# Kernel optimization log

Measured on AMD Instinct MI355X. Metric: run time of the kernel, lower is better.

The kernel has to match this reference:

```python
import jax, jax.numpy as jnp
import numpy as np

B, N, C, H = 4, 1024, 1024, 16
HD = C // H  # 64
THETA = 10000.0


def _rope_cos_sin(n, hd, theta):
    # classic 1D RoPE cache; [n, hd] with each freq repeated twice (interleaved pairs)
    inv_freq = 1.0 / theta ** (jnp.arange(0, hd, 2, dtype=jnp.float32) / hd)
    t = jnp.arange(n, dtype=jnp.float32)
    freqs = t[:, None] * inv_freq[None, :]              # [n, hd/2]
    cos = jnp.repeat(jnp.cos(freqs), 2, axis=-1)        # [n, hd]
    sin = jnp.repeat(jnp.sin(freqs), 2, axis=-1)
    # original clones & forces row 0 to identity rotation (already true since t=0)
    cos = cos.at[0].set(1.0)
    sin = sin.at[0].set(0.0)
    return cos, sin


def _rotate_half(x):
    # interleaved rotate-half: (x0,x1,x2,x3,...) -> (-x1,x0,-x3,x2,...)
    x1 = x[..., 0::2]
    x2 = x[..., 1::2]
    return jnp.stack((-x2, x1), axis=-1).reshape(x.shape)


def setup_inputs() -> dict:
    key = jax.random.key(0)
    ks = jax.random.split(key, 5)
    s = 0.02
    return {
        "x": jax.random.normal(ks[0], (B, N, C), dtype=jnp.float32),
        "qkv_w": jax.random.normal(ks[1], (3 * C, C), dtype=jnp.float32) * s,
        "qkv_b": jax.random.normal(ks[2], (3 * C,), dtype=jnp.float32) * s,
        "proj_w": jax.random.normal(ks[3], (C, C), dtype=jnp.float32) * s,
        "proj_b": jax.random.normal(ks[4], (C,), dtype=jnp.float32) * s,
    }


def reference(x, qkv_w, qkv_b, proj_w, proj_b):
    b, n, c = x.shape
    h, hd = H, HD
    qkv = x @ qkv_w.T + qkv_b                              # [b, n, 3c]
    qkv = qkv.reshape(b, n, 3, h, hd).transpose(2, 0, 3, 1, 4)  # [3, b, h, n, hd]
    q, k, v = qkv[0], qkv[1], qkv[2]
    scale = hd ** -0.5
    q = q * scale                                          # explicit pre-scale (as in source)
    cos, sin = _rope_cos_sin(n, hd, THETA)                 # [n, hd]
    cos = cos[None, None]                                  # broadcast over b, h
    sin = sin[None, None]
    q = q * cos + _rotate_half(q) * sin
    k = k * cos + _rotate_half(k) * sin
    # F.scaled_dot_product_attention also applies its default 1/sqrt(hd) scale
    logits = jnp.einsum('bhqd,bhkd->bhqk', q, k) * scale   # [b, h, n, n]
    attn = jax.nn.softmax(logits, axis=-1)
    out = jnp.einsum('bhqk,bhkd->bhqd', attn, v)           # [b, h, n, hd]
    out = out.transpose(0, 2, 1, 3).reshape(b, n, c)
    return out @ proj_w.T + proj_b
```

## Files before the change

### kernel.cpp

```cpp
#include <hip/hip_runtime.h>
#include <hip/hip_bf16.h>
#include <stdint.h>

#define DEVI __device__ __forceinline__

typedef __attribute__((ext_vector_type(8))) short short8;
typedef __attribute__((ext_vector_type(4))) short short4v;
typedef __attribute__((ext_vector_type(4))) float floatx4;

DEVI ushort f2bf(float f) {
  union { float f; uint32_t u; } v; v.f = f;
  uint32_t u = v.u;
  uint32_t r = (u + 0x7FFFu + ((u >> 16) & 1u)) >> 16;
  return (ushort)r;
}
DEVI ushort f2bf_fast(float f) {
  union { float f; uint32_t u; } v; v.f = f;
  return (ushort)((v.u + 0x8000u) >> 16);
}
DEVI float bf2f(ushort h) {
  union { uint32_t u; float f; } v; v.u = ((uint32_t)h) << 16;
  return v.f;
}
DEVI void gld_lds16(const void* g, void* l) {
  __builtin_amdgcn_global_load_lds(
      (const __attribute__((address_space(1))) unsigned int*)g,
      (__attribute__((address_space(3))) unsigned int*)l, 16, 0, 0);
}

__global__ __launch_bounds__(256, 4) void cast_all(
    const float* __restrict__ x, const float* __restrict__ w1,
    const float* __restrict__ w2, ushort* __restrict__ xb,
    ushort* __restrict__ w1b, ushort* __restrict__ w2b,
    float2* __restrict__ tab) {
  const int N1 = 4096 * 1024, N2 = 3072 * 1024, N3 = 1024 * 1024;
  int id = blockIdx.x * 256 + threadIdx.x;
  if (id < 32768) {
    int j = id & 31, n = id >> 5;
    float inv = powf(10000.0f, -(float)(2 * j) / 64.0f);
    float fr = (float)n * inv;
    tab[id] = make_float2(cosf(fr), sinf(fr));
  }
  int i = id * 4;
  const int total = N1 + N2 + N3;
  int stride = gridDim.x * 256 * 4;
  for (; i < total; i += stride) {
    const float* src; ushort* dst; int off;
    if (i < N1) { src = x; dst = xb; off = i; }
    else if (i < N1 + N2) { src = w1; dst = w1b; off = i - N1; }
    else { src = w2; dst = w2b; off = i - N1 - N2; }
    float4 v = *(const float4*)(src + off);
    ushort4 o;
    o.x = f2bf(v.x); o.y = f2bf(v.y); o.z = f2bf(v.z); o.w = f2bf(v.w);
    *(ushort4*)(dst + off) = o;
  }
}

__global__ __launch_bounds__(256, 4) void gemm_qkv(
    const ushort* __restrict__ A, const ushort* __restrict__ Bm,
    const float* __restrict__ bias, const float2* __restrict__ tab,
    ushort* __restrict__ Qb, ushort* __restrict__ Kb,
    ushort* __restrict__ Vsrc) {
  __shared__ __align__(16) char As[2][8192];
  __shared__ __align__(16) char Bs[2][8192];
  const int tid = threadIdx.x;
  const int w = tid >> 6, lane = tid & 63;

  const int bid = blockIdx.x;
  const int xcd = bid & 7, i5 = bid >> 3;
  const int lm = i5 & 7, ln = i5 >> 3;
  const int mt = (xcd & 3) * 8 + lm;
  const int nt = (xcd >> 2) * 12 + ln;
  const int m0 = mt * 128, n0 = nt * 128;

  const int wm = (w >> 1) * 64, wn = (w & 1) * 64;
  const int lrow = lane & 15, g = lane >> 4;
  const int swrd = (g ^ ((lrow >> 1) & 3)) << 4;

  const int swsrc = (((lane & 3) ^ ((lane >> 3) & 3)) << 4);
  const char* aG = (const char*)A + (size_t)(m0 + w * 32 + (lane >> 2)) * 2048 + swsrc;
  const char* bG = (const char*)Bm + (size_t)(n0 + w * 32 + (lane >> 2)) * 2048 + swsrc;
  const int ldst = w * 2048 + lane * 16;

  auto STAGE = [&](const int buf) {
    gld_lds16(aG, &As[buf][0] + ldst);
    gld_lds16(aG + 16 * 2048, &As[buf][0] + ldst + 1024);
    gld_lds16(bG, &Bs[buf][0] + ldst);
    gld_lds16(bG + 16 * 2048, &Bs[buf][0] + ldst + 1024);
    aG += 64; bG += 64;
  };

  floatx4 acc[4][4] = {};

  auto TILE = [&](const int buf) {
    short8 af[4], bf[4];
#pragma unroll
    for (int t = 0; t < 4; ++t) {
      af[t] = *(const short8*)(&As[buf][0] + (wm + t * 16 + lrow) * 64 + swrd);
      bf[t] = *(const short8*)(&Bs[buf][0] + (wn + t * 16 + lrow) * 64 + swrd);
    }
#pragma unroll
    for (int i = 0; i < 4; ++i)
#pragma unroll
      for (int j = 0; j < 4; ++j)
        acc[i][j] = __builtin_amdgcn_mfma_f32_16x16x32_bf16(af[i], bf[j], acc[i][j], 0, 0, 0);
  };

  STAGE(0);
  asm volatile("s_waitcnt vmcnt(0)" ::: "memory");
  __builtin_amdgcn_s_barrier();
  __builtin_amdgcn_sched_barrier(0);

  for (int t = 0; t < 32; t += 2) {
    STAGE(1);
    __builtin_amdgcn_sched_barrier(0);
    TILE(0);
    asm volatile("s_waitcnt vmcnt(0)" ::: "memory");
    __builtin_amdgcn_s_barrier();
    __builtin_amdgcn_sched_barrier(0);

    if (t + 2 < 32) STAGE(0);
    __builtin_amdgcn_sched_barrier(0);
    TILE(1);
    asm volatile("s_waitcnt vmcnt(0)" ::: "memory");
    __builtin_amdgcn_s_barrier();
    __builtin_amdgcn_sched_barrier(0);
  }

  const int role = n0 >> 10;
  const float sc = (1.0f / 64.0f) * 1.44269504088896f;
#pragma unroll
  for (int i = 0; i < 4; ++i) {
    int mrow = m0 + wm + i * 16 + (lane >> 4) * 4;
#pragma unroll
    for (int j = 0; j < 4; ++j) {
      int ncol = n0 + wn + j * 16 + (lane & 15);
      float bv = bias[ncol];
      int cm = ncol & 1023;
      int h = cm >> 6, d = cm & 63;
#pragma unroll
      for (int r = 0; r < 4; ++r) {
        float v = acc[i][j][r] + bv;
        int row = mrow + r;
        int b = row >> 10, n = row & 1023;
        if (role == 2) {
          Vsrc[(size_t)row * 1024 + cm] = f2bf(v);
        } else {
          float p = __shfl_xor(v, 1);
          float2 cs = tab[n * 32 + (d >> 1)];
          float o = (d & 1) ? (v * cs.x + p * cs.y) : (v * cs.x - p * cs.y);
          if (role == 0) o *= sc;
          ushort* dst = (role == 0) ? Qb : Kb;
          dst[((size_t)(b * 16 + h) * 1024 + n) * 64 + d] = f2bf(o);
        }
      }
    }
  }
}

__global__ __launch_bounds__(256, 3) void gemm_proj(
    const ushort* __restrict__ A, const ushort* __restrict__ Bm,
    const float* __restrict__ bias, float* __restrict__ Cout) {
  __shared__ __align__(16) char lds[3][16384];
  char* L0 = &lds[0][0];
  const int tid = threadIdx.x;
  const int w = tid >> 6, lane = tid & 63;

  const int bid = blockIdx.x;
  const int xcd = bid & 7, i5 = bid >> 3;
  const int lm = i5 & 7, ln = i5 >> 3;
  const int mt = (xcd & 3) * 8 + lm;
  const int nt = (xcd >> 2) * 4 + ln;
  const int m0 = mt * 128, n0 = nt * 128;

  const int wm = (w >> 1) * 64, wn = (w & 1) * 64;
  const int lrow = lane & 15, g = lane >> 4;
  const int swrd = (g ^ ((lrow >> 1) & 3)) << 4;

  const int swsrc = (((lane & 3) ^ ((lane >> 3) & 3)) << 4);
  const char* aG = (const char*)A + (size_t)(m0 + w * 32 + (lane >> 2)) * 2048 + swsrc;
  const char* bG = (const char*)Bm + (size_t)(n0 + w * 32 + (lane >> 2)) * 2048 + swsrc;
  const int ldst = w * 2048 + lane * 16;

  auto STAGE = [&](const int base) {
    char* L = L0 + base;
    gld_lds16(aG, L + ldst);
    gld_lds16(aG + 16 * 2048, L + ldst + 1024);
    gld_lds16(bG, L + 8192 + ldst);
    gld_lds16(bG + 16 * 2048, L + 8192 + ldst + 1024);
    aG += 64; bG += 64;
  };

  floatx4 acc[4][4] = {};

  auto TILE = [&](const int base) {
    const char* L = L0 + base;
    short8 af[4], bf[4];
#pragma unroll
    for (int t = 0; t < 4; ++t) {
      af[t] = *(const short8*)(L + (wm + t * 16 + lrow) * 64 + swrd);
      bf[t] = *(const short8*)(L + 8192 + (wn + t * 16 + lrow) * 64 + swrd);
    }
#pragma unroll
    for (int i = 0; i < 4; ++i)
#pragma unroll
      for (int j = 0; j < 4; ++j)
        acc[i][j] = __builtin_amdgcn_mfma_f32_16x16x32_bf16(af[i], bf[j], acc[i][j], 0, 0, 0);
  };

  STAGE(0);
  STAGE(16384);
  int bT = 0, bS = 32768;

  for (int t = 0; t < 31; ++t) {
    asm volatile("s_waitcnt vmcnt(4)" ::: "memory");
    __builtin_amdgcn_s_barrier();
    __builtin_amdgcn_sched_barrier(0);
    if (t < 30) STAGE(bS);
    __builtin_amdgcn_sched_barrier(0);
    TILE(bT);
    __builtin_amdgcn_sched_barrier(0);
    bT += 16384; if (bT == 49152) bT = 0;
    bS += 16384; if (bS == 49152) bS = 0;
  }
  asm volatile("s_waitcnt vmcnt(0)" ::: "memory");
  __builtin_amdgcn_s_barrier();
  __builtin_amdgcn_sched_barrier(0);
  TILE(bT);

#pragma unroll
  for (int i = 0; i < 4; ++i) {
    int mrow = m0 + wm + i * 16 + (lane >> 4) * 4;
#pragma unroll
    for (int j = 0; j < 4; ++j) {
      int ncol = n0 + wn + j * 16 + (lane & 15);
      float bv = bias[ncol];
#pragma unroll
      for (int r = 0; r < 4; ++r)
        Cout[(size_t)(mrow + r) * 1024 + ncol] = acc[i][j][r] + bv;
    }
  }
}

__global__ __launch_bounds__(256, 4) void v_trans(
    const ushort* __restrict__ Vsrc, ushort* __restrict__ Vt) {
  __shared__ ushort t[64][72];
  int bh = blockIdx.y, ntile = blockIdx.x;
  int b = bh >> 4, h = bh & 15;
  int n0 = ntile * 64;
  int tid = threadIdx.x;
  int r = tid >> 2, cc = (tid & 3) * 16;
  const ushort* src = Vsrc + (size_t)(b * 1024 + n0 + r) * 1024 + h * 64 + cc;
  *(short8*)(&t[r][cc]) = *(const short8*)(src);
  *(short8*)(&t[r][cc + 8]) = *(const short8*)(src + 8);
  __syncthreads();
  int d = tid >> 2;
  ushort outv[16];
#pragma unroll
  for (int i = 0; i < 16; ++i) outv[i] = t[cc + i][d];
  ushort* dst = Vt + (size_t)bh * 65536 + (size_t)d * 1024 + n0 + cc;
  *(short8*)(dst) = *(const short8*)(outv);
  *(short8*)(dst + 8) = *(const short8*)(outv + 8);
}

__global__ __launch_bounds__(256, 4) void attn(
    const ushort* __restrict__ Q, const ushort* __restrict__ Kc,
    const ushort* __restrict__ Vt, ushort* __restrict__ AO) {
  __shared__ char lds[2][16384];
  char* ldsbase = &lds[0][0];
  int id = blockIdx.x;
  int bh = id & 63, qi = id >> 6;
  int b = bh >> 4, h = bh & 15;
  int q0 = qi * 64;
  int tid = threadIdx.x, w = tid >> 6, lane = tid & 63;
  int l15 = lane & 15, g = lane >> 4;
  const ushort* Qbh = Q + (size_t)bh * 65536;
  const char* Kbh = (const char*)(Kc + (size_t)bh * 65536);
  const char* Vbh = (const char*)(Vt + (size_t)bh * 65536);

  short8 qf[2];
#pragma unroll
  for (int ks = 0; ks < 2; ++ks)
    qf[ks] = *(const short8*)(Qbh + (size_t)(q0 + w * 16 + l15) * 64 + ks * 32 + g * 8);

  int kaddr[8];
#pragma unroll
  for (int ks = 0; ks < 2; ++ks)
#pragma unroll
    for (int nt = 0; nt < 4; ++nt) {
      int row = nt * 16 + l15;
      kaddr[ks * 4 + nt] = (row * 128 + ks * 64 + g * 16) ^ ((row & 7) << 4);
    }
  int vaddr[16];
#pragma unroll
  for (int ch = 0; ch < 2; ++ch)
#pragma unroll
    for (int dt = 0; dt < 4; ++dt)
#pragma unroll
      for (int hf = 0; hf < 2; ++hf) {
        int row = dt * 16 + l15;
        vaddr[(ch * 4 + dt) * 2 + hf] =
            8192 + ((row * 128 + ch * 64 + hf * 32 + g * 8) ^ ((row & 7) << 4));
      }

  const int d0 = w * 2048 + lane * 16;
  const int d1 = d0 + 1024;
  const int r0 = d0 >> 7, r1 = d1 >> 7;
  const int s0 = d0 ^ ((r0 & 7) << 4), s1 = d1 ^ ((r1 & 7) << 4);
  const char* pK0 = Kbh + s0;
  const char* pK1 = Kbh + s1;
  const char* pV0 = Vbh + r0 * 2048 + (s0 & 127);
  const char* pV1 = Vbh + r1 * 2048 + (s1 & 127);

  auto STAGE = [&](const int B) {
    gld_lds16(pK0, ldsbase + B + d0);
    gld_lds16(pK1, ldsbase + B + d1);
    gld_lds16(pV0, ldsbase + B + 8192 + d0);
    gld_lds16(pV1, ldsbase + B + 8192 + d1);
    pK0 += 8192; pK1 += 8192; pV0 += 128; pV1 += 128;
  };

  floatx4 oacc[4] = {};
  float lrun = 0.f;

  auto TILE = [&](const int B) {
    floatx4 sacc[4] = {};
    __builtin_amdgcn_s_setprio(1);
#pragma unroll
    for (int ks = 0; ks < 2; ++ks) {
      short8 kf[4];
#pragma unroll
      for (int nt = 0; nt < 4; ++nt)
        kf[nt] = *(const short8*)(ldsbase + B + kaddr[ks * 4 + nt]);
#pragma unroll
      for (int nt = 0; nt < 4; ++nt)
        sacc[nt] = __builtin_amdgcn_mfma_f32_16x16x32_bf16(kf[nt], qf[ks], sacc[nt], 0, 0, 0);
    }
    __builtin_amdgcn_s_setprio(0);

    float rs = 0.f;
#pragma unroll
    for (int nt = 0; nt < 4; ++nt)
#pragma unroll
      for (int r = 0; r < 4; ++r) {
        float p = __builtin_amdgcn_exp2f(sacc[nt][r]);
        sacc[nt][r] = p;
        rs += p;
      }
    lrun += rs;

    short8 pa[2];
#pragma unroll
    for (int ch = 0; ch < 2; ++ch)
#pragma unroll
      for (int r = 0; r < 4; ++r) {
        pa[ch][r] = (short)f2bf_fast(sacc[2 * ch][r]);
        pa[ch][r + 4] = (short)f2bf_fast(sacc[2 * ch + 1][r]);
      }

    __builtin_amdgcn_s_setprio(1);
#pragma unroll
    for (int ch = 0; ch < 2; ++ch)
#pragma unroll
      for (int dt = 0; dt < 4; ++dt) {
        short4v va = *(const short4v*)(ldsbase + B + vaddr[(ch * 4 + dt) * 2]);
        short4v vb = *(const short4v*)(ldsbase + B + vaddr[(ch * 4 + dt) * 2 + 1]);
        short8 vf = __builtin_shufflevector(va, vb, 0, 1, 2, 3, 4, 5, 6, 7);
        oacc[dt] = __builtin_amdgcn_mfma_f32_16x16x32_bf16(pa[ch], vf, oacc[dt], 0, 0, 0);
      }
    __builtin_amdgcn_s_setprio(0);
  };

  STAGE(0);
  asm volatile("s_waitcnt vmcnt(0)" ::: "memory");
  __builtin_amdgcn_s_barrier();
  __builtin_amdgcn_sched_barrier(0);

  for (int kt = 0; kt < 16; kt += 2) {
    STAGE(16384);
    __builtin_amdgcn_sched_barrier(0);
    TILE(0);
    asm volatile("s_waitcnt vmcnt(0)" ::: "memory");
    __builtin_amdgcn_s_barrier();
    __builtin_amdgcn_sched_barrier(0);

    if (kt + 2 < 16) STAGE(0);
    __builtin_amdgcn_sched_barrier(0);
    TILE(16384);
    asm volatile("s_waitcnt vmcnt(0)" ::: "memory");
    __builtin_amdgcn_s_barrier();
    __builtin_amdgcn_sched_barrier(0);
  }

  lrun += __shfl_xor(lrun, 16);
  lrun += __shfl_xor(lrun, 32);
  float linv = 1.0f / lrun;
  float linvR[4];
#pragma unroll
  for (int r = 0; r < 4; ++r) linvR[r] = __shfl(linv, g * 4 + r);
#pragma unroll
  for (int r = 0; r < 4; ++r) {
    int nseq = q0 + w * 16 + g * 4 + r;
#pragma unroll
    for (int dt = 0; dt < 4; ++dt) {
      int d = dt * 16 + l15;
      AO[(size_t)(b * 1024 + nseq) * 1024 + h * 64 + d] = f2bf(oacc[dt][r] * linvR[r]);
    }
  }
}

extern "C" void kernel_launch(void* const* d_in, const int* in_sizes, int n_in,
                              void* d_out, int out_size, void* d_ws, size_t ws_size,
                              hipStream_t stream) {
  const float* x = (const float*)d_in[0];
  const float* qkv_w = (const float*)d_in[1];
  const float* qkv_b = (const float*)d_in[2];
  const float* proj_w = (const float*)d_in[3];
  const float* proj_b = (const float*)d_in[4];
  float* out = (float*)d_out;

  char* ws = (char*)d_ws;
  size_t off = 0;
  auto alloc = [&](size_t bytes) -> void* {
    void* p = ws + off;
    off += (bytes + 255) & ~(size_t)255;
    return p;
  };
  ushort* xb = (ushort*)alloc(4096ull * 1024 * 2);
  ushort* wqkvb = (ushort*)alloc(3072ull * 1024 * 2);
  ushort* wprojb = (ushort*)alloc(1024ull * 1024 * 2);
  ushort* Qb = (ushort*)alloc(64ull * 1024 * 64 * 2);
  ushort* Kb = (ushort*)alloc(64ull * 1024 * 64 * 2);
  ushort* Vsrc = (ushort*)alloc(4096ull * 1024 * 2);
  ushort* Vt = (ushort*)alloc(64ull * 1024 * 64 * 2);
  ushort* AO = (ushort*)alloc(4096ull * 1024 * 2);
  float2* tab = (float2*)alloc(1024ull * 32 * sizeof(float2));

  cast_all<<<2048, 256, 0, stream>>>(x, qkv_w, proj_w, xb, wqkvb, wprojb, tab);

  gemm_qkv<<<768, 256, 0, stream>>>(xb, wqkvb, qkv_b, tab, Qb, Kb, Vsrc);

  dim3 gv(16, 64);
  v_trans<<<gv, 256, 0, stream>>>(Vsrc, Vt);

  attn<<<1024, 256, 0, stream>>>(Qb, Kb, Vt, AO);

  gemm_proj<<<256, 256, 0, stream>>>(AO, wprojb, proj_b, out);
}
```

Baseline: 97.89 us.

## Fuse V transpose into QKV GEMM epilogue via LDS staging

The V-role tiles of the QKV GEMM now stage bias-added bf16 results in a shared-memory tile and write them out transposed into the per-head Vt layout. The separate v_trans kernel and the Vsrc intermediate buffer are removed. This saves one kernel launch plus an 8 MB write-and-read round trip through global memory. In exchange the GEMM's shared-memory footprint grows to about 33 KB, which may reduce occupancy under the 4-blocks launch bound, and the V blocks gain an extra barrier.

```diff
diff --git a/kernel.cpp b/kernel.cpp
--- a/kernel.cpp
+++ b/kernel.cpp
@@ -60,9 +60,10 @@
     const ushort* __restrict__ A, const ushort* __restrict__ Bm,
     const float* __restrict__ bias, const float2* __restrict__ tab,
     ushort* __restrict__ Qb, ushort* __restrict__ Kb,
-    ushort* __restrict__ Vsrc) {
-  __shared__ __align__(16) char As[2][8192];
-  __shared__ __align__(16) char Bs[2][8192];
+    ushort* __restrict__ Vt) {
+  __shared__ __align__(16) char pool[33792];
+  char* AsP = pool;
+  char* BsP = pool + 16384;
   const int tid = threadIdx.x;
   const int w = tid >> 6, lane = tid & 63;
 
@@ -83,10 +84,10 @@
   const int ldst = w * 2048 + lane * 16;
 
   auto STAGE = [&](const int buf) {
-    gld_lds16(aG, &As[buf][0] + ldst);
-    gld_lds16(aG + 16 * 2048, &As[buf][0] + ldst + 1024);
-    gld_lds16(bG, &Bs[buf][0] + ldst);
-    gld_lds16(bG + 16 * 2048, &Bs[buf][0] + ldst + 1024);
+    gld_lds16(aG, AsP + buf * 8192 + ldst);
+    gld_lds16(aG + 16 * 2048, AsP + buf * 8192 + ldst + 1024);
+    gld_lds16(bG, BsP + buf * 8192 + ldst);
+    gld_lds16(bG + 16 * 2048, BsP + buf * 8192 + ldst + 1024);
     aG += 64; bG += 64;
   };
 
@@ -96,8 +97,8 @@
     short8 af[4], bf[4];
 #pragma unroll
     for (int t = 0; t < 4; ++t) {
-      af[t] = *(const short8*)(&As[buf][0] + (wm + t * 16 + lrow) * 64 + swrd);
-      bf[t] = *(const short8*)(&Bs[buf][0] + (wn + t * 16 + lrow) * 64 + swrd);
+      af[t] = *(const short8*)(AsP + buf * 8192 + (wm + t * 16 + lrow) * 64 + swrd);
+      bf[t] = *(const short8*)(BsP + buf * 8192 + (wn + t * 16 + lrow) * 64 + swrd);
     }
 #pragma unroll
     for (int i = 0; i < 4; ++i)
@@ -128,30 +129,53 @@
   }
 
   const int role = n0 >> 10;
-  const float sc = (1.0f / 64.0f) * 1.44269504088896f;
-#pragma unroll
-  for (int i = 0; i < 4; ++i) {
-    int mrow = m0 + wm + i * 16 + (lane >> 4) * 4;
-#pragma unroll
-    for (int j = 0; j < 4; ++j) {
-      int ncol = n0 + wn + j * 16 + (lane & 15);
-      float bv = bias[ncol];
-      int cm = ncol & 1023;
-      int h = cm >> 6, d = cm & 63;
-#pragma unroll
-      for (int r = 0; r < 4; ++r) {
-        float v = acc[i][j][r] + bv;
-        int row = mrow + r;
-        int b = row >> 10, n = row & 1023;
-        if (role == 2) {
-          Vsrc[(size_t)row * 1024 + cm] = f2bf(v);
-        } else {
+  if (role == 2) {
+    char* T = pool;
+#pragma unroll
+    for (int i = 0; i < 4; ++i) {
+      int lr0 = wm + i * 16 + g * 4;
+#pragma unroll
+      for (int j = 0; j < 4; ++j) {
+        int lc = wn + j * 16 + lrow;
+        float bv = bias[n0 + lc];
+        ushort4 o;
+#pragma unroll
+        for (int r = 0; r < 4; ++r) ((ushort*)&o)[r] = f2bf(acc[i][j][r] + bv);
+        *(ushort4*)(T + lc * 264 + lr0 * 2) = o;
+      }
+    }
+    __syncthreads();
+    const int b = m0 >> 10, nbase = m0 & 1023;
+    const int h0 = (n0 - 2048) >> 6;
+    const int c = tid >> 1, half = tid & 1;
+    const int h = h0 + (c >> 6), d = c & 63;
+    ushort* dst = Vt + (size_t)(b * 16 + h) * 65536 + (size_t)d * 1024 + nbase + half * 64;
+    const char* src = T + c * 264 + half * 128;
+#pragma unroll
+    for (int k = 0; k < 16; ++k)
+      *(short4v*)(dst + k * 4) = *(const short4v*)(src + k * 8);
+  } else {
+    const float sc = (1.0f / 64.0f) * 1.44269504088896f;
+#pragma unroll
+    for (int i = 0; i < 4; ++i) {
+      int mrow = m0 + wm + i * 16 + g * 4;
+#pragma unroll
+      for (int j = 0; j < 4; ++j) {
+        int ncol = n0 + wn + j * 16 + lrow;
+        float bv = bias[ncol];
+        int cm = ncol & 1023;
+        int h = cm >> 6, d = cm & 63;
+#pragma unroll
+        for (int r = 0; r < 4; ++r) {
+          float v = acc[i][j][r] + bv;
+          int row = mrow + r;
+          int b = row >> 10, n = row & 1023;
           float p = __shfl_xor(v, 1);
           float2 cs = tab[n * 32 + (d >> 1)];
           float o = (d & 1) ? (v * cs.x + p * cs.y) : (v * cs.x - p * cs.y);
           if (role == 0) o *= sc;
-          ushort* dst = (role == 0) ? Qb : Kb;
-          dst[((size_t)(b * 16 + h) * 1024 + n) * 64 + d] = f2bf(o);
+          ushort* dstqk = (role == 0) ? Qb : Kb;
+          dstqk[((size_t)(b * 16 + h) * 1024 + n) * 64 + d] = f2bf(o);
         }
       }
     }
@@ -240,27 +264,6 @@
         Cout[(size_t)(mrow + r) * 1024 + ncol] = acc[i][j][r] + bv;
     }
   }
-}
-
-__global__ __launch_bounds__(256, 4) void v_trans(
-    const ushort* __restrict__ Vsrc, ushort* __restrict__ Vt) {
-  __shared__ ushort t[64][72];
-  int bh = blockIdx.y, ntile = blockIdx.x;
-  int b = bh >> 4, h = bh & 15;
-  int n0 = ntile * 64;
-  int tid = threadIdx.x;
-  int r = tid >> 2, cc = (tid & 3) * 16;
-  const ushort* src = Vsrc + (size_t)(b * 1024 + n0 + r) * 1024 + h * 64 + cc;
-  *(short8*)(&t[r][cc]) = *(const short8*)(src);
-  *(short8*)(&t[r][cc + 8]) = *(const short8*)(src + 8);
-  __syncthreads();
-  int d = tid >> 2;
-  ushort outv[16];
-#pragma unroll
-  for (int i = 0; i < 16; ++i) outv[i] = t[cc + i][d];
-  ushort* dst = Vt + (size_t)bh * 65536 + (size_t)d * 1024 + n0 + cc;
-  *(short8*)(dst) = *(const short8*)(outv);
-  *(short8*)(dst + 8) = *(const short8*)(outv + 8);
 }
 
 __global__ __launch_bounds__(256, 4) void attn(
@@ -431,17 +434,13 @@
   ushort* wprojb = (ushort*)alloc(1024ull * 1024 * 2);
   ushort* Qb = (ushort*)alloc(64ull * 1024 * 64 * 2);
   ushort* Kb = (ushort*)alloc(64ull * 1024 * 64 * 2);
-  ushort* Vsrc = (ushort*)alloc(4096ull * 1024 * 2);
   ushort* Vt = (ushort*)alloc(64ull * 1024 * 64 * 2);
   ushort* AO = (ushort*)alloc(4096ull * 1024 * 2);
   float2* tab = (float2*)alloc(1024ull * 32 * sizeof(float2));
 
   cast_all<<<2048, 256, 0, stream>>>(x, qkv_w, proj_w, xb, wqkvb, wprojb, tab);
 
-  gemm_qkv<<<768, 256, 0, stream>>>(xb, wqkvb, qkv_b, tab, Qb, Kb, Vsrc);
-
-  dim3 gv(16, 64);
-  v_trans<<<gv, 256, 0, stream>>>(Vsrc, Vt);
+  gemm_qkv<<<768, 256, 0, stream>>>(xb, wqkvb, qkv_b, tab, Qb, Kb, Vt);
 
   attn<<<1024, 256, 0, stream>>>(Qb, Kb, Vt, AO);
 
```

After: 86.02 us. -12.1%, faster.
